# Kernel tuning notes

Hardware: AMD Instinct MI355X
Metric: run time of the kernel (lower is better)

Reference implementation:

```python
import jax, jax.numpy as jnp
import numpy as np

B, N_IN, N_MFS, N_RULES = 8192, 8, 4, 2048


def setup_inputs() -> dict:
    key = jax.random.key(0)
    k1, k2 = jax.random.split(key)
    # fuzzified membership values in [0, 1): (n_cases, n_in, n_mfs)
    x = jax.random.uniform(k1, (B, N_IN, N_MFS), dtype=jnp.float32)
    # rule MF-index table: values in [-1, n_mfs-1]; -1 means 'variable unused in rule'
    mf_indices = jax.random.randint(k2, (N_RULES, N_IN), 0, N_MFS + 1, dtype=jnp.int32) - 1
    return {"x": x, "mf_indices": mf_indices}


def reference(x, mf_indices):
    """AntecedentLayer.forward, rules path with AND_p (product t-norm).
    x:          (B, n_in, n_mfs)
    mf_indices: (n_rules, n_in), -1 = masked
    returns fire strengths: (B, n_rules)
    """
    cond = mf_indices == -1                      # (R, n_in)
    safe_idx = jnp.where(cond, 0, mf_indices)    # clamp sentinel for gather
    n_in = x.shape[1]
    # ants[b, r, i] = x[b, i, safe_idx[r, i]]  -> (B, R, n_in)
    ants = x[:, jnp.arange(n_in)[None, :], safe_idx]
    # masked variables contribute identity (1.0) to the product t-norm
    ants = jnp.where(cond[None, :, :], jnp.float32(1.0), ants)
    return jnp.prod(ants, axis=2)                # (B, R)
```

## Files before the change

### kernel.cpp

```cpp
#include <hip/hip_runtime.h>

#define B        8192
#define N_IN     8
#define N_MFS    4
#define N_RULES  2048

#define THREADS  256
#define NB       8
#define LUT_STRIDE 104

__global__ void pack_rules(const int* __restrict__ mf, unsigned int* __restrict__ pk) {
    int r = blockIdx.x * blockDim.x + threadIdx.x;
    if (r >= N_RULES) return;
    unsigned int v = 0;
#pragma unroll
    for (int p = 0; p < 4; ++p) {
        int ia = mf[r * N_IN + 2 * p];
        int ib = mf[r * N_IN + 2 * p + 1];
        unsigned int a = (ia < 0) ? 4u : (unsigned int)ia;
        unsigned int b = (ib < 0) ? 4u : (unsigned int)ib;
        unsigned int byte = 4u * (a * 5u + b);
        v |= byte << (8 * p);
    }
    pk[r] = v;
}

__device__ __forceinline__ float rule_val(const char* lut_bytes, unsigned int pk) {
    float v0 = *(const float*)(lut_bytes +   0 + (pk & 0xFFu));
    float v1 = *(const float*)(lut_bytes + 100 + ((pk >> 8) & 0xFFu));
    float v2 = *(const float*)(lut_bytes + 200 + ((pk >> 16) & 0xFFu));
    float v3 = *(const float*)(lut_bytes + 300 + (pk >> 24));
    return (v0 * v1) * (v2 * v3);
}

__global__ __launch_bounds__(THREADS) void fire_kernel(
        const float* __restrict__ x,
        const unsigned int* __restrict__ pk,
        float* __restrict__ out) {
    __shared__ unsigned int srules[N_RULES];
    __shared__ float slut[NB * LUT_STRIDE];

    const int tid = threadIdx.x;
    const int b0  = blockIdx.x * NB;

    {
        const uint4* g4 = (const uint4*)pk;
        uint4* s4 = (uint4*)srules;
#pragma unroll
        for (int i = tid; i < N_RULES / 4; i += THREADS) s4[i] = g4[i];
    }

    for (int e = tid; e < NB * 100; e += THREADS) {
        int bl   = e / 100;
        int rest = e - bl * 100;
        int p    = rest / 25;
        int c    = rest - p * 25;
        int a    = c / 5;
        int bb   = c - a * 5;
        const float* xb = x + (size_t)(b0 + bl) * (N_IN * N_MFS);
        float va = (a  < 4) ? xb[(2 * p)     * N_MFS + a ] : 1.0f;
        float vb = (bb < 4) ? xb[(2 * p + 1) * N_MFS + bb] : 1.0f;
        slut[bl * LUT_STRIDE + rest] = va * vb;
    }
    __syncthreads();

#pragma unroll 1
    for (int bl = 0; bl < NB; ++bl) {
        const char* lutb = (const char*)(slut + bl * LUT_STRIDE);
        float* orow = out + (size_t)(b0 + bl) * N_RULES;
#pragma unroll
        for (int pass = 0; pass < 2; ++pass) {
            int r0 = pass * (THREADS * 4) + tid * 4;
            uint4 pkt = *(const uint4*)&srules[r0];
            float4 res;
            res.x = rule_val(lutb, pkt.x);
            res.y = rule_val(lutb, pkt.y);
            res.z = rule_val(lutb, pkt.z);
            res.w = rule_val(lutb, pkt.w);
            *(float4*)&orow[r0] = res;
        }
    }
}

extern "C" void kernel_launch(void* const* d_in, const int* in_sizes, int n_in,
                              void* d_out, int out_size, void* d_ws, size_t ws_size,
                              hipStream_t stream) {
    const float* x  = (const float*)d_in[0];
    const int*   mf = (const int*)d_in[1];
    float* out = (float*)d_out;
    unsigned int* pk = (unsigned int*)d_ws;

    pack_rules<<<(N_RULES + THREADS - 1) / THREADS, THREADS, 0, stream>>>(mf, pk);
    fire_kernel<<<B / NB, THREADS, 0, stream>>>(x, pk, out);
}
```

Before: 95.56 us.

## Fuse rule packing into fire kernel and keep precomputed LDS addresses in registers

Drops the separate pack_rules launch. Each thread now reads its own 8 rules' MF indices straight from global memory and precomputes 32 LDS byte addresses held in registers. The shared rule table is removed, the batch-row loop is fully unrolled, and the LUT stride becomes 101 floats to vary bank mapping. This removes one kernel launch and the per-row shared-memory rule reads, at the cost of much higher register pressure and every block re-reading the whole mf table from global or L2.

```diff
diff --git a/kernel.cpp b/kernel.cpp
--- a/kernel.cpp
+++ b/kernel.cpp
@@ -7,77 +7,72 @@
 
 #define THREADS  256
 #define NB       8
-#define LUT_STRIDE 104
-
-__global__ void pack_rules(const int* __restrict__ mf, unsigned int* __restrict__ pk) {
-    int r = blockIdx.x * blockDim.x + threadIdx.x;
-    if (r >= N_RULES) return;
-    unsigned int v = 0;
-#pragma unroll
-    for (int p = 0; p < 4; ++p) {
-        int ia = mf[r * N_IN + 2 * p];
-        int ib = mf[r * N_IN + 2 * p + 1];
-        unsigned int a = (ia < 0) ? 4u : (unsigned int)ia;
-        unsigned int b = (ib < 0) ? 4u : (unsigned int)ib;
-        unsigned int byte = 4u * (a * 5u + b);
-        v |= byte << (8 * p);
-    }
-    pk[r] = v;
-}
-
-__device__ __forceinline__ float rule_val(const char* lut_bytes, unsigned int pk) {
-    float v0 = *(const float*)(lut_bytes +   0 + (pk & 0xFFu));
-    float v1 = *(const float*)(lut_bytes + 100 + ((pk >> 8) & 0xFFu));
-    float v2 = *(const float*)(lut_bytes + 200 + ((pk >> 16) & 0xFFu));
-    float v3 = *(const float*)(lut_bytes + 300 + (pk >> 24));
-    return (v0 * v1) * (v2 * v3);
-}
+#define LUT_W    101
 
 __global__ __launch_bounds__(THREADS) void fire_kernel(
         const float* __restrict__ x,
-        const unsigned int* __restrict__ pk,
-        float* __restrict__ out) {
-    __shared__ unsigned int srules[N_RULES];
-    __shared__ float slut[NB * LUT_STRIDE];
+        const int*   __restrict__ mf,
+        float* __restrict__ out)
+{
+    __shared__ float slut[NB * LUT_W];
 
     const int tid = threadIdx.x;
     const int b0  = blockIdx.x * NB;
 
-    {
-        const uint4* g4 = (const uint4*)pk;
-        uint4* s4 = (uint4*)srules;
+    const char* lds_base = (const char*)slut;
+    const char* ap[2][4][4];
 #pragma unroll
-        for (int i = tid; i < N_RULES / 4; i += THREADS) s4[i] = g4[i];
+    for (int pass = 0; pass < 2; ++pass) {
+#pragma unroll
+        for (int j = 0; j < 4; ++j) {
+            const int r = pass * (THREADS * 4) + tid * 4 + j;
+            const int4* mr = (const int4*)(mf + r * N_IN);
+            const int4 lo = mr[0];
+            const int4 hi = mr[1];
+            const int idx[8] = {lo.x, lo.y, lo.z, lo.w, hi.x, hi.y, hi.z, hi.w};
+#pragma unroll
+            for (int p = 0; p < 4; ++p) {
+                const unsigned int a = idx[2*p]   < 0 ? 4u : (unsigned int)idx[2*p];
+                const unsigned int b = idx[2*p+1] < 0 ? 4u : (unsigned int)idx[2*p+1];
+                ap[pass][j][p] = lds_base + (p * 100u + 4u * (a * 5u + b));
+            }
+        }
     }
 
     for (int e = tid; e < NB * 100; e += THREADS) {
-        int bl   = e / 100;
-        int rest = e - bl * 100;
-        int p    = rest / 25;
-        int c    = rest - p * 25;
-        int a    = c / 5;
-        int bb   = c - a * 5;
+        const int bl   = e / 100;
+        const int rest = e - bl * 100;
+        const int p    = rest / 25;
+        const int c    = rest - p * 25;
+        const int a    = c / 5;
+        const int bb   = c - a * 5;
         const float* xb = x + (size_t)(b0 + bl) * (N_IN * N_MFS);
-        float va = (a  < 4) ? xb[(2 * p)     * N_MFS + a ] : 1.0f;
-        float vb = (bb < 4) ? xb[(2 * p + 1) * N_MFS + bb] : 1.0f;
-        slut[bl * LUT_STRIDE + rest] = va * vb;
+        const float va = (a  < 4) ? xb[(2*p)   * N_MFS + a ] : 1.0f;
+        const float vb = (bb < 4) ? xb[(2*p+1) * N_MFS + bb] : 1.0f;
+        slut[bl * LUT_W + rest] = va * vb;
     }
     __syncthreads();
 
-#pragma unroll 1
+#pragma unroll
     for (int bl = 0; bl < NB; ++bl) {
-        const char* lutb = (const char*)(slut + bl * LUT_STRIDE);
-        float* orow = out + (size_t)(b0 + bl) * N_RULES;
+        const unsigned int lo = bl * (LUT_W * 4);
 #pragma unroll
         for (int pass = 0; pass < 2; ++pass) {
-            int r0 = pass * (THREADS * 4) + tid * 4;
-            uint4 pkt = *(const uint4*)&srules[r0];
             float4 res;
-            res.x = rule_val(lutb, pkt.x);
-            res.y = rule_val(lutb, pkt.y);
-            res.z = rule_val(lutb, pkt.z);
-            res.w = rule_val(lutb, pkt.w);
-            *(float4*)&orow[r0] = res;
+            float* o = out + (size_t)(b0 + bl) * N_RULES + pass * (THREADS * 4) + tid * 4;
+#pragma unroll
+            for (int j = 0; j < 4; ++j) {
+                const float v0 = *(const float*)(ap[pass][j][0] + lo);
+                const float v1 = *(const float*)(ap[pass][j][1] + lo);
+                const float v2 = *(const float*)(ap[pass][j][2] + lo);
+                const float v3 = *(const float*)(ap[pass][j][3] + lo);
+                const float r  = (v0 * v1) * (v2 * v3);
+                if (j == 0) res.x = r;
+                else if (j == 1) res.y = r;
+                else if (j == 2) res.z = r;
+                else res.w = r;
+            }
+            *(float4*)o = res;
         }
     }
 }
@@ -88,8 +83,7 @@
     const float* x  = (const float*)d_in[0];
     const int*   mf = (const int*)d_in[1];
     float* out = (float*)d_out;
-    unsigned int* pk = (unsigned int*)d_ws;
+    (void)d_ws; (void)ws_size;
 
-    pack_rules<<<(N_RULES + THREADS - 1) / THREADS, THREADS, 0, stream>>>(mf, pk);
-    fire_kernel<<<B / NB, THREADS, 0, stream>>>(x, pk, out);
+    fire_kernel<<<B / NB, THREADS, 0, stream>>>(x, mf, out);
 }
```

Result: faster. 84.40 us (-11.7%).
